# Performance work log

Measured on AMD Instinct MI355X. Metric: run time of the kernel, lower is better.

The kernel has to match this reference:

```python
import jax, jax.numpy as jnp
import numpy as np

EPS = 1e-6

# config matching the torch module: ctx != 'object_ord', bp == 'sgmn', tracker=False, opt='add'

def setup_inputs() -> dict:
    bs, nseq, num_box, num_ctx, max_len = 32, 24, 196, 196, 6
    key = jax.random.key(0)
    ks = jax.random.split(key, 8)
    ent_attn = jax.random.normal(ks[0], (bs, nseq, num_box), dtype=jnp.float32)
    spo_attn = jax.random.normal(ks[1], (bs, nseq, num_box, num_ctx), dtype=jnp.float32)
    ctx_idx_adjusted = jax.random.randint(ks[2], (bs, num_box, num_ctx), 0, num_box, dtype=jnp.int32)
    cls_raw = jax.random.randint(ks[3], (bs, num_box), 0, 100, dtype=jnp.int32)
    roi_cls = jnp.where(cls_raw < 90, cls_raw, -1)
    roi_mask = (jax.random.uniform(ks[4], (bs, num_box, num_ctx)) < 0.9).astype(jnp.float32)
    weight_on_children = jax.random.uniform(ks[5], (bs, nseq, num_box), dtype=jnp.float32)
    traversal_lists = jax.random.randint(ks[6], (bs, max_len), 0, nseq, dtype=jnp.int32)
    adj_raw = jax.random.randint(ks[7], (bs, nseq, nseq), 0, 2 * nseq, dtype=jnp.int32)
    adj_matrices = jnp.where(adj_raw < nseq, adj_raw, -1)
    return {
        'traversal_lists': traversal_lists,
        'adj_matrices': adj_matrices,
        'ent_attn': ent_attn,
        'spo_attn': spo_attn,
        'ctx_idx_adjusted': ctx_idx_adjusted,
        'roi_cls': roi_cls,
        'roi_mask': roi_mask,
        'weight_on_children': weight_on_children,
    }


def _bottom_up(traversal_lists, adj_matrices, ent_attn, spo_attn,
               ctx_idx_adjusted, roi_cls, roi_mask, weight_on_children):
    bs, nseq, num_box = ent_attn.shape
    k_cls = (roi_cls != -1).astype(ent_attn.dtype)           # [bs, num_box]
    batch_ix = jnp.arange(bs)
    # per-batch gather: child_atn[b, j, ctx[b, i, c]]
    gather_ctx = jax.vmap(lambda ca, ci: ca[:, ci])           # ([nseq,nb],[nb,nc]) -> [nseq,nb,nc]

    def step(ea, p):  # p: [bs] parent ids for this traversal step
        valid_p = p >= 0
        pc = jnp.maximum(p, 0)
        # edge ids from parent row of adjacency: [bs, nseq]
        edges = jnp.take_along_axis(adj_matrices, pc[:, None, None], axis=1)[:, 0]
        cmask = (edges >= 0) & valid_p[:, None]               # which columns are real children
        cm = cmask.astype(ea.dtype)
        ec = jnp.maximum(edges, 0)
        # children attention, zeroed for non-children and invalid ROI classes
        child_atn = ea * cm[:, :, None] * k_cls[:, None, :]   # [bs, nseq, num_box]
        # gather "child could be context c of box i" scores
        gathered = gather_ctx(child_atn, ctx_idx_adjusted)    # [bs, nseq, num_box, num_ctx]
        fmask = roi_mask[:, None] * cm[:, :, None, None]      # filter_mask per child row
        sc = gathered * fmask                                 # k_scores_children_be_any_ctx
        rel = jnp.take_along_axis(spo_attn, ec[:, :, None, None], axis=1)
        sr = rel * fmask * k_cls[:, None, :, None]            # k_scores_rel_by_any_edge
        # sgmn transfer: sum over ctx dim (extra roi_mask multiply as in torch)
        core = jnp.sum(sc * sr * roi_mask[:, None], axis=-1)  # [bs, nseq, num_box]
        nch = jnp.sum(cm, axis=1)                             # [bs]
        neff = jnp.maximum(nch, 1.0)                          # dummy child when no children
        add_to_sub = jnp.sum(core, axis=1) + neff[:, None] * EPS  # opt='add' -> sum over children
        sub_atn = jnp.take_along_axis(ea, pc[:, None, None], axis=1)[:, 0]        # [bs, num_box]
        w = jnp.take_along_axis(weight_on_children, pc[:, None, None], axis=1)[:, 0]
        upd = sub_atn + add_to_sub * w
        # NormAttnMap('cossim'): divide by detached max |.| clipped at 1
        norm = jax.lax.stop_gradient(jnp.max(jnp.abs(upd), axis=-1, keepdims=True))
        norm = jnp.where(norm <= 1.0, 1.0, norm)
        upd = upd / norm
        upd = jnp.where(roi_cls == -1, -1.0, upd)             # opt='add' branch sets -1
        write = valid_p & (nch > 0)                           # bs_mask
        new_row = jnp.where(write[:, None], upd, sub_atn)
        ea = ea.at[batch_ix, pc].set(new_row)
        return ea, None

    ea, _ = jax.lax.scan(step, ent_attn, traversal_lists.T)
    return ea


def reference(traversal_lists, adj_matrices, ent_attn, spo_attn,
              ctx_idx_adjusted, roi_cls, roi_mask, weight_on_children):
    return _bottom_up(traversal_lists, adj_matrices, ent_attn, spo_attn,
                      ctx_idx_adjusted, roi_cls, roi_mask, weight_on_children)
```

## Files before the change

### kernel.cpp

```cpp
#include <hip/hip_runtime.h>

#define NSEQ   24
#define NBOX   196
#define NCTX   196
#define MAXLEN 6
#define EPSV   1e-6f

#define TILES      25
#define K1_THREADS 512
#define K1_WAVES   8

__global__ __launch_bounds__(K1_THREADS) void step_compute(
    const float* __restrict__ src,
    float*       __restrict__ ea_copy,
    const float* __restrict__ spo,
    const int*   __restrict__ ctx,
    const int*   __restrict__ roi_cls,
    const float* __restrict__ rm,
    const int*   __restrict__ trav,
    const int*   __restrict__ adj,
    float*       __restrict__ add_raw,
    int step, int do_copy)
{
    const int b    = blockIdx.x / TILES;
    const int tile = blockIdx.x % TILES;
    const int tid  = threadIdx.x;

    __shared__ __align__(16) float cae[NSEQ][NBOX];
    __shared__ int   s_childE[NSEQ + 1];
    __shared__ int   s_childJ[NSEQ];
    __shared__ int   s_nch;

    if (do_copy) {
        const int total4 = 32 * NSEQ * NBOX / 4;
        int idx = blockIdx.x * K1_THREADS + tid;
        if (idx < total4)
            ((float4*)ea_copy)[idx] = ((const float4*)src)[idx];
    }

    const int p = trav[b * MAXLEN + step];
    if (tid == 0) {
        int n = 0;
        if (p >= 0) {
            const int* arow = adj + ((size_t)b * NSEQ + p) * NSEQ;
            for (int j = 0; j < NSEQ; ++j) {
                int e = arow[j];
                if (e >= 0) { s_childJ[n] = j; s_childE[n] = e; ++n; }
            }
        }
        if (n > 0) s_childE[n] = s_childE[0];
        s_nch = n;
    }
    __syncthreads();
    const int nch = s_nch;
    if (nch == 0) return;

    {
        const int items = nch * (NBOX / 4);
        const int4* roi4 = (const int4*)(roi_cls + b * NBOX);
        for (int t = tid; t < items; t += K1_THREADS) {
            int n = t / (NBOX / 4);
            int q = t - n * (NBOX / 4);
            float4 e4 = ((const float4*)(src + ((size_t)b * NSEQ + s_childJ[n]) * NBOX))[q];
            int4   r4 = roi4[q];
            float4 v;
            v.x = (r4.x != -1) ? e4.x : 0.0f;
            v.y = (r4.y != -1) ? e4.y : 0.0f;
            v.z = (r4.z != -1) ? e4.z : 0.0f;
            v.w = (r4.w != -1) ? e4.w : 0.0f;
            ((float4*)&cae[n][0])[q] = v;
        }
    }
    __syncthreads();

    const int  wave = tid >> 6;
    const int  lane = tid & 63;
    const int  i    = tile * K1_WAVES + wave;
    if (i >= NBOX) return;

    float acc = 0.0f;
    const bool act = lane < 49;
    if (act) {
        const size_t bi = (size_t)b * NBOX + i;
        const int4   idx4 = ((const int4*)  (ctx + bi * NCTX))[lane];
        const float4 m4   = ((const float4*)(rm  + bi * NCTX))[lane];
        const float* sbase = spo + ((size_t)b * NSEQ * NBOX + i) * NCTX;

        float4 a4 = make_float4(0.f, 0.f, 0.f, 0.f);
        float4 s4 = ((const float4*)(sbase + (size_t)s_childE[0] * NBOX * NCTX))[lane];
        for (int n = 0; n < nch; ++n) {
            float4 nx = ((const float4*)(sbase + (size_t)s_childE[n + 1] * NBOX * NCTX))[lane];
            a4.x = fmaf(m4.x * cae[n][idx4.x], s4.x, a4.x);
            a4.y = fmaf(m4.y * cae[n][idx4.y], s4.y, a4.y);
            a4.z = fmaf(m4.z * cae[n][idx4.z], s4.z, a4.z);
            a4.w = fmaf(m4.w * cae[n][idx4.w], s4.w, a4.w);
            s4 = nx;
        }
        acc = (a4.x + a4.y) + (a4.z + a4.w);
    }
    #pragma unroll
    for (int off = 32; off >= 1; off >>= 1)
        acc += __shfl_down(acc, off, 64);
    if (lane == 0) {
        float kci = (roi_cls[b * NBOX + i] != -1) ? 1.0f : 0.0f;
        add_raw[b * NBOX + i] = kci * acc;
    }
}

__global__ __launch_bounds__(256) void step_finalize(
    float*       __restrict__ ea,
    const float* __restrict__ add_raw,
    const float* __restrict__ wc,
    const int*   __restrict__ roi_cls,
    const int*   __restrict__ trav,
    const int*   __restrict__ adj,
    int step)
{
    const int b   = blockIdx.x;
    const int tid = threadIdx.x;
    const int p   = trav[b * MAXLEN + step];

    int nch = 0;
    if (p >= 0) {
        const int* arow = adj + ((size_t)b * NSEQ + p) * NSEQ;
        for (int j = 0; j < NSEQ; ++j) nch += (arow[j] >= 0) ? 1 : 0;
    }
    if (p < 0 || nch == 0) return;

    float upd = 0.0f, a = 0.0f;
    if (tid < NBOX) {
        const float sub = ea[((size_t)b * NSEQ + p) * NBOX + tid];
        const float w   = wc[((size_t)b * NSEQ + p) * NBOX + tid];
        upd = sub + (add_raw[b * NBOX + tid] + (float)nch * EPSV) * w;
        a = fabsf(upd);
    }
    #pragma unroll
    for (int off = 32; off >= 1; off >>= 1)
        a = fmaxf(a, __shfl_down(a, off, 64));
    __shared__ float wmax[4];
    if ((tid & 63) == 0) wmax[tid >> 6] = a;
    __syncthreads();
    float norm = fmaxf(fmaxf(wmax[0], wmax[1]), fmaxf(wmax[2], wmax[3]));
    norm = (norm <= 1.0f) ? 1.0f : norm;
    if (tid < NBOX) {
        float val = upd / norm;
        if (roi_cls[b * NBOX + tid] == -1) val = -1.0f;
        ea[((size_t)b * NSEQ + p) * NBOX + tid] = val;
    }
}

extern "C" void kernel_launch(void* const* d_in, const int* in_sizes, int n_in,
                              void* d_out, int out_size, void* d_ws, size_t ws_size,
                              hipStream_t stream) {
    const int*   trav = (const int*)  d_in[0];
    const int*   adj  = (const int*)  d_in[1];
    const float* ent  = (const float*)d_in[2];
    const float* spo  = (const float*)d_in[3];
    const int*   ctx  = (const int*)  d_in[4];
    const int*   roi  = (const int*)  d_in[5];
    const float* rm   = (const float*)d_in[6];
    const float* wc   = (const float*)d_in[7];

    float* ea      = (float*)d_out;
    float* add_raw = (float*)d_ws;

    const int bs = in_sizes[0] / MAXLEN;

    for (int t = 0; t < MAXLEN; ++t) {
        step_compute<<<bs * TILES, K1_THREADS, 0, stream>>>(
            t == 0 ? ent : ea, ea, spo, ctx, roi, rm, trav, adj, add_raw,
            t, t == 0 ? 1 : 0);
        step_finalize<<<bs, 256, 0, stream>>>(
            ea, add_raw, wc, roi, trav, adj, t);
    }
}
```

Baseline: 105.1 us.

## Fuse per-step finalize into next step's compute kernel with double-buffered workspace

Folds the normalization/finalize of step t-1 into the step t compute kernel. Every tile recomputes the previous parent row's update redundantly, and tile 0 writes it back. Child rows that equal the previous parent come from shared memory, so the kernel never reads a row that is still being written. This cuts the launch count from 12 to 7 and uses ping-pong workspace buffers to avoid races. The spo prefetch is also deepened from one to three iterations ahead, at the cost of redundant per-block finalize work and hardcoded batch size.

Result: slower. 115.7 us (+10.0%).

```diff
diff --git a/kernel.cpp b/kernel.cpp
--- a/kernel.cpp
+++ b/kernel.cpp
@@ -5,41 +5,54 @@
 #define NCTX   196
 #define MAXLEN 6
 #define EPSV   1e-6f
+#define BS     32
 
 #define TILES      25
 #define K1_THREADS 512
-#define K1_WAVES   8
-
-__global__ __launch_bounds__(K1_THREADS) void step_compute(
-    const float* __restrict__ src,
-    float*       __restrict__ ea_copy,
+#define NB4        (NBOX / 4)
+
+#define WS_ARAW(buf)  ((buf) * BS * NBOX)
+#define WS_OLD(buf)   ((2 + (buf)) * BS * NBOX)
+
+__global__ __launch_bounds__(K1_THREADS) void step_fused(
+    const float* __restrict__ ent,
+    float*       __restrict__ ea,
     const float* __restrict__ spo,
     const int*   __restrict__ ctx,
     const int*   __restrict__ roi_cls,
     const float* __restrict__ rm,
+    const float* __restrict__ wc,
     const int*   __restrict__ trav,
     const int*   __restrict__ adj,
-    float*       __restrict__ add_raw,
-    int step, int do_copy)
+    float*       __restrict__ ws,
+    int step)
 {
     const int b    = blockIdx.x / TILES;
     const int tile = blockIdx.x % TILES;
     const int tid  = threadIdx.x;
+    const float* state = (step == 0) ? ent : ea;
+
+    float*       araw_w = ws + WS_ARAW(step & 1);
+    const float* araw_r = ws + WS_ARAW((step ^ 1) & 1);
+    float*       old_w  = ws + WS_OLD(step & 1);
+    const float* old_r  = ws + WS_OLD((step ^ 1) & 1);
 
     __shared__ __align__(16) float cae[NSEQ][NBOX];
-    __shared__ int   s_childE[NSEQ + 1];
+    __shared__ __align__(16) float s_fin[NBOX];
+    __shared__ float s_upd[NBOX];
+    __shared__ float s_red[8];
+    __shared__ int   s_childE[NSEQ + 3];
     __shared__ int   s_childJ[NSEQ];
-    __shared__ int   s_nch;
-
-    if (do_copy) {
-        const int total4 = 32 * NSEQ * NBOX / 4;
+    __shared__ int   s_scal[5];
+
+    if (step == 0) {
+        const int total4 = BS * NSEQ * NBOX / 4;
         int idx = blockIdx.x * K1_THREADS + tid;
-        if (idx < total4)
-            ((float4*)ea_copy)[idx] = ((const float4*)src)[idx];
-    }
-
-    const int p = trav[b * MAXLEN + step];
+        if (idx < total4) ((float4*)ea)[idx] = ((const float4*)ent)[idx];
+    }
+
     if (tid == 0) {
+        const int p = trav[b * MAXLEN + step];
         int n = 0;
         if (p >= 0) {
             const int* arow = adj + ((size_t)b * NSEQ + p) * NSEQ;
@@ -48,21 +61,67 @@
                 if (e >= 0) { s_childJ[n] = j; s_childE[n] = e; ++n; }
             }
         }
-        if (n > 0) s_childE[n] = s_childE[0];
-        s_nch = n;
-    }
-    __syncthreads();
-    const int nch = s_nch;
+        int c0 = (n > 0) ? s_childE[0] : 0;
+        s_childE[n] = c0; s_childE[n + 1] = c0; s_childE[n + 2] = c0;
+        int pp = -1, np = 0;
+        if (step > 0) {
+            pp = trav[b * MAXLEN + step - 1];
+            if (pp >= 0) {
+                const int* arow = adj + ((size_t)b * NSEQ + pp) * NSEQ;
+                for (int j = 0; j < NSEQ; ++j) np += (arow[j] >= 0) ? 1 : 0;
+            }
+        }
+        s_scal[0] = n; s_scal[1] = p; s_scal[2] = pp; s_scal[3] = np;
+        s_scal[4] = (step > 0 && pp >= 0 && np > 0) ? 1 : 0;
+    }
+    __syncthreads();
+    const int nch = s_scal[0], p = s_scal[1], p_prev = s_scal[2],
+              nch_prev = s_scal[3], use_fin = s_scal[4];
+
+    float a = 0.0f;
+    if (use_fin && tid < NBOX) {
+        float old = old_r[b * NBOX + tid];
+        float w   = wc[((size_t)b * NSEQ + p_prev) * NBOX + tid];
+        float u   = old + (araw_r[b * NBOX + tid] + (float)nch_prev * EPSV) * w;
+        s_upd[tid] = u;
+        a = fabsf(u);
+    }
+    #pragma unroll
+    for (int off = 32; off >= 1; off >>= 1) a = fmaxf(a, __shfl_down(a, off, 64));
+    if ((tid & 63) == 0) s_red[tid >> 6] = a;
+    __syncthreads();
+    if (use_fin && tid < NBOX) {
+        float norm = fmaxf(fmaxf(fmaxf(s_red[0], s_red[1]), fmaxf(s_red[2], s_red[3])),
+                           fmaxf(fmaxf(s_red[4], s_red[5]), fmaxf(s_red[6], s_red[7])));
+        norm = (norm <= 1.0f) ? 1.0f : norm;
+        float v = s_upd[tid] / norm;
+        if (roi_cls[b * NBOX + tid] == -1) v = -1.0f;
+        s_fin[tid] = v;
+    }
+    __syncthreads();
+
+    if (tile == 0 && tid < NBOX) {
+        if (use_fin) ea[((size_t)b * NSEQ + p_prev) * NBOX + tid] = s_fin[tid];
+        if (p >= 0) {
+            float v = (use_fin && p == p_prev)
+                      ? s_fin[tid]
+                      : state[((size_t)b * NSEQ + p) * NBOX + tid];
+            old_w[b * NBOX + tid] = v;
+        }
+    }
+
     if (nch == 0) return;
 
     {
-        const int items = nch * (NBOX / 4);
+        const int items = nch * NB4;
         const int4* roi4 = (const int4*)(roi_cls + b * NBOX);
         for (int t = tid; t < items; t += K1_THREADS) {
-            int n = t / (NBOX / 4);
-            int q = t - n * (NBOX / 4);
-            float4 e4 = ((const float4*)(src + ((size_t)b * NSEQ + s_childJ[n]) * NBOX))[q];
-            int4   r4 = roi4[q];
+            int n = t / NB4, q = t - n * NB4;
+            int j = s_childJ[n];
+            float4 e4 = (use_fin && j == p_prev)
+                        ? ((const float4*)s_fin)[q]
+                        : ((const float4*)(state + ((size_t)b * NSEQ + j) * NBOX))[q];
+            int4 r4 = roi4[q];
             float4 v;
             v.x = (r4.x != -1) ? e4.x : 0.0f;
             v.y = (r4.y != -1) ? e4.y : 0.0f;
@@ -73,70 +132,69 @@
     }
     __syncthreads();
 
-    const int  wave = tid >> 6;
-    const int  lane = tid & 63;
-    const int  i    = tile * K1_WAVES + wave;
+    const int wave = tid >> 6, lane = tid & 63;
+    const int i = tile * 8 + wave;
     if (i >= NBOX) return;
 
     float acc = 0.0f;
-    const bool act = lane < 49;
-    if (act) {
+    if (lane < NB4) {
         const size_t bi = (size_t)b * NBOX + i;
         const int4   idx4 = ((const int4*)  (ctx + bi * NCTX))[lane];
         const float4 m4   = ((const float4*)(rm  + bi * NCTX))[lane];
-        const float* sbase = spo + ((size_t)b * NSEQ * NBOX + i) * NCTX;
+        const float* sb = spo + ((size_t)b * NSEQ * NBOX + i) * NCTX;
+        const size_t stride = (size_t)NBOX * NCTX;
 
         float4 a4 = make_float4(0.f, 0.f, 0.f, 0.f);
-        float4 s4 = ((const float4*)(sbase + (size_t)s_childE[0] * NBOX * NCTX))[lane];
+        float4 s0 = ((const float4*)(sb + (size_t)s_childE[0] * stride))[lane];
+        float4 s1 = ((const float4*)(sb + (size_t)s_childE[1] * stride))[lane];
+        float4 s2 = ((const float4*)(sb + (size_t)s_childE[2] * stride))[lane];
         for (int n = 0; n < nch; ++n) {
-            float4 nx = ((const float4*)(sbase + (size_t)s_childE[n + 1] * NBOX * NCTX))[lane];
-            a4.x = fmaf(m4.x * cae[n][idx4.x], s4.x, a4.x);
-            a4.y = fmaf(m4.y * cae[n][idx4.y], s4.y, a4.y);
-            a4.z = fmaf(m4.z * cae[n][idx4.z], s4.z, a4.z);
-            a4.w = fmaf(m4.w * cae[n][idx4.w], s4.w, a4.w);
-            s4 = nx;
+            float4 nx = ((const float4*)(sb + (size_t)s_childE[n + 3] * stride))[lane];
+            a4.x = fmaf(m4.x * cae[n][idx4.x], s0.x, a4.x);
+            a4.y = fmaf(m4.y * cae[n][idx4.y], s0.y, a4.y);
+            a4.z = fmaf(m4.z * cae[n][idx4.z], s0.z, a4.z);
+            a4.w = fmaf(m4.w * cae[n][idx4.w], s0.w, a4.w);
+            s0 = s1; s1 = s2; s2 = nx;
         }
         acc = (a4.x + a4.y) + (a4.z + a4.w);
     }
     #pragma unroll
-    for (int off = 32; off >= 1; off >>= 1)
-        acc += __shfl_down(acc, off, 64);
+    for (int off = 32; off >= 1; off >>= 1) acc += __shfl_down(acc, off, 64);
     if (lane == 0) {
         float kci = (roi_cls[b * NBOX + i] != -1) ? 1.0f : 0.0f;
-        add_raw[b * NBOX + i] = kci * acc;
+        araw_w[b * NBOX + i] = kci * acc;
     }
 }
 
-__global__ __launch_bounds__(256) void step_finalize(
+__global__ __launch_bounds__(256) void tail_finalize(
     float*       __restrict__ ea,
-    const float* __restrict__ add_raw,
+    const float* __restrict__ ws,
     const float* __restrict__ wc,
     const int*   __restrict__ roi_cls,
     const int*   __restrict__ trav,
-    const int*   __restrict__ adj,
-    int step)
+    const int*   __restrict__ adj)
 {
-    const int b   = blockIdx.x;
-    const int tid = threadIdx.x;
-    const int p   = trav[b * MAXLEN + step];
-
+    const int b = blockIdx.x, tid = threadIdx.x;
+    const int last = MAXLEN - 1;
+    const float* araw = ws + WS_ARAW(last & 1);
+    const float* oldr = ws + WS_OLD(last & 1);
+    const int p = trav[b * MAXLEN + last];
     int nch = 0;
     if (p >= 0) {
-        const int* arow = adj + ((size_t)b * NSEQ + p) * NSEQ;
-        for (int j = 0; j < NSEQ; ++j) nch += (arow[j] >= 0) ? 1 : 0;
+        const int* ar = adj + ((size_t)b * NSEQ + p) * NSEQ;
+        for (int j = 0; j < NSEQ; ++j) nch += (ar[j] >= 0) ? 1 : 0;
     }
     if (p < 0 || nch == 0) return;
 
     float upd = 0.0f, a = 0.0f;
     if (tid < NBOX) {
-        const float sub = ea[((size_t)b * NSEQ + p) * NBOX + tid];
-        const float w   = wc[((size_t)b * NSEQ + p) * NBOX + tid];
-        upd = sub + (add_raw[b * NBOX + tid] + (float)nch * EPSV) * w;
+        float old = oldr[b * NBOX + tid];
+        float w   = wc[((size_t)b * NSEQ + p) * NBOX + tid];
+        upd = old + (araw[b * NBOX + tid] + (float)nch * EPSV) * w;
         a = fabsf(upd);
     }
     #pragma unroll
-    for (int off = 32; off >= 1; off >>= 1)
-        a = fmaxf(a, __shfl_down(a, off, 64));
+    for (int off = 32; off >= 1; off >>= 1) a = fmaxf(a, __shfl_down(a, off, 64));
     __shared__ float wmax[4];
     if ((tid & 63) == 0) wmax[tid >> 6] = a;
     __syncthreads();
@@ -161,16 +219,12 @@
     const float* rm   = (const float*)d_in[6];
     const float* wc   = (const float*)d_in[7];
 
-    float* ea      = (float*)d_out;
-    float* add_raw = (float*)d_ws;
-
-    const int bs = in_sizes[0] / MAXLEN;
+    float* ea = (float*)d_out;
+    float* ws = (float*)d_ws;
 
     for (int t = 0; t < MAXLEN; ++t) {
-        step_compute<<<bs * TILES, K1_THREADS, 0, stream>>>(
-            t == 0 ? ent : ea, ea, spo, ctx, roi, rm, trav, adj, add_raw,
-            t, t == 0 ? 1 : 0);
-        step_finalize<<<bs, 256, 0, stream>>>(
-            ea, add_raw, wc, roi, trav, adj, t);
-    }
+        step_fused<<<BS * TILES, K1_THREADS, 0, stream>>>(
+            ent, ea, spo, ctx, roi, rm, wc, trav, adj, ws, t);
+    }
+    tail_finalize<<<BS, 256, 0, stream>>>(ea, ws, wc, roi, trav, adj);
 }
```
